# Performance work log

Measured on AMD Instinct MI355X. Metric: run time of the kernel, lower is better.

## Reference

```python
import jax, jax.numpy as jnp
import numpy as np

N_NODES = 50000
N_EDGES = 500000
D_FEAT = 128
OUT_CLASSES = 64


def setup_inputs() -> dict:
    key = jax.random.key(0)
    k_h, k_src, k_dst, k_w, k_b = jax.random.split(key, 5)
    h = jax.random.normal(k_h, (N_NODES, D_FEAT), dtype=jnp.float32)
    src = jax.random.randint(k_src, (N_EDGES,), 0, N_NODES, dtype=jnp.int64)
    dst = jax.random.randint(k_dst, (N_EDGES,), 0, N_NODES, dtype=jnp.int64)
    # nn.Linear(in_features*2, out_classes): weight [out, 2*in], bias [out]
    W = jax.random.normal(k_w, (OUT_CLASSES, 2 * D_FEAT), dtype=jnp.float32) * (1.0 / np.sqrt(2 * D_FEAT))
    b = jax.random.normal(k_b, (OUT_CLASSES,), dtype=jnp.float32) * 0.01
    return {"h": h, "src": src, "dst": dst, "W": W, "b": b}


def reference(h, src, dst, W, b):
    # Gather per-edge endpoint features, concat along feature dim, linear score.
    # Equivalent to torch: self.W(torch.cat([h[src], h[dst]], 1))
    h_u = h[src]                # [E, D]
    h_v = h[dst]                # [E, D]
    # Split W into src/dst halves to avoid materializing the concat:
    W_u, W_v = W[:, :D_FEAT], W[:, D_FEAT:]
    score = h_u @ W_u.T + h_v @ W_v.T + b   # [E, out_classes]
    return score
```

## Files before the change

kernel.cpp:

```cpp
#include <hip/hip_runtime.h>
#include <stdint.h>
#include <stddef.h>

constexpr int kNodes = 50000;
constexpr int kEdges = 500000;
constexpr int kD     = 128;
constexpr int kC     = 64;
constexpr int kK     = 256;

typedef __attribute__((ext_vector_type(8))) short  short8;
typedef __attribute__((ext_vector_type(4))) float  floatx4;

__device__ __forceinline__ unsigned short f2bf(float f) {
  union { float f; unsigned u; } v; v.f = f;
  unsigned u = v.u;
  unsigned r = u + 0x7FFFu + ((u >> 16) & 1u);
  return (unsigned short)(r >> 16);
}

__device__ __forceinline__ float bf2f(short s) {
  union { unsigned u; float f; } v;
  v.u = ((unsigned)(unsigned short)s) << 16;
  return v.f;
}

__device__ __forceinline__ short8 cvt8(floatx4 a, floatx4 b) {
  short8 r;
  r[0] = (short)f2bf(a[0]); r[1] = (short)f2bf(a[1]);
  r[2] = (short)f2bf(a[2]); r[3] = (short)f2bf(a[3]);
  r[4] = (short)f2bf(b[0]); r[5] = (short)f2bf(b[1]);
  r[6] = (short)f2bf(b[2]); r[7] = (short)f2bf(b[3]);
  return r;
}

__global__ __launch_bounds__(256)
void node_gemm_kernel(const float* __restrict__ h,
                      const float* __restrict__ W,
                      const float* __restrict__ b,
                      unsigned short* __restrict__ Pu,
                      unsigned short* __restrict__ Pv) {
  __shared__ short8 Blds[2048];

  const int tid = threadIdx.x;

  for (int s = tid; s < 2048; s += 256) {
    int kstep = s >> 9;
    int ntile = (s >> 6) & 7;
    int ln    = s & 63;
    int np = ntile * 16 + (ln & 15);
    int k  = kstep * 32 + (ln >> 4) * 8;
    int wc = (np < kC) ? np : (np - kC);
    int wk = (np < kC) ? k  : (k + kD);
    const float* wp = W + wc * kK + wk;
    Blds[s] = cvt8(*reinterpret_cast<const floatx4*>(wp),
                   *reinterpret_cast<const floatx4*>(wp + 4));
  }

  const int lane = tid & 63;
  const int wave = tid >> 6;
  const int rowA = lane & 15;
  const int quad = lane >> 4;
  const int col  = rowA;

  const int rowbase = blockIdx.x * 128 + wave * 32;
  int n0 = rowbase + rowA;       if (n0 >= kNodes) n0 = kNodes - 1;
  int n1 = rowbase + 16 + rowA;  if (n1 >= kNodes) n1 = kNodes - 1;

  short8 a0[4], a1[4];
#pragma unroll
  for (int kstep = 0; kstep < 4; ++kstep) {
    const float* p0 = h + (size_t)n0 * kD + kstep * 32 + quad * 8;
    const float* p1 = h + (size_t)n1 * kD + kstep * 32 + quad * 8;
    a0[kstep] = cvt8(__builtin_nontemporal_load(reinterpret_cast<const floatx4*>(p0)),
                     __builtin_nontemporal_load(reinterpret_cast<const floatx4*>(p0 + 4)));
    a1[kstep] = cvt8(__builtin_nontemporal_load(reinterpret_cast<const floatx4*>(p1)),
                     __builtin_nontemporal_load(reinterpret_cast<const floatx4*>(p1 + 4)));
  }

  floatx4 acc0[8], acc1[8];
#pragma unroll
  for (int nt = 0; nt < 8; ++nt) {
    acc0[nt] = (floatx4){0.f, 0.f, 0.f, 0.f};
    acc1[nt] = (floatx4){0.f, 0.f, 0.f, 0.f};
  }

  __syncthreads();

#pragma unroll
  for (int kstep = 0; kstep < 4; ++kstep) {
#pragma unroll
    for (int nt = 0; nt < 8; ++nt) {
      short8 bfrag = Blds[(kstep * 8 + nt) * 64 + lane];
      acc0[nt] = __builtin_amdgcn_mfma_f32_16x16x32_bf16(a0[kstep], bfrag,
                                                         acc0[nt], 0, 0, 0);
      acc1[nt] = __builtin_amdgcn_mfma_f32_16x16x32_bf16(a1[kstep], bfrag,
                                                         acc1[nt], 0, 0, 0);
    }
  }

  const bool full = (rowbase + 32) <= kNodes;
#pragma unroll
  for (int nt = 0; nt < 4; ++nt) {
    float bv = b[nt * 16 + col];
#pragma unroll
    for (int r = 0; r < 4; ++r) {
      int ra = rowbase + quad * 4 + r;
      int rb = ra + 16;
      if (full || ra < kNodes)
        Pu[(size_t)ra * kC + nt * 16 + col] = f2bf(acc0[nt][r] + bv);
      if (full || rb < kNodes)
        Pu[(size_t)rb * kC + nt * 16 + col] = f2bf(acc1[nt][r] + bv);
    }
  }
#pragma unroll
  for (int nt = 4; nt < 8; ++nt) {
#pragma unroll
    for (int r = 0; r < 4; ++r) {
      int ra = rowbase + quad * 4 + r;
      int rb = ra + 16;
      if (full || ra < kNodes)
        Pv[(size_t)ra * kC + (nt - 4) * 16 + col] = f2bf(acc0[nt][r]);
      if (full || rb < kNodes)
        Pv[(size_t)rb * kC + (nt - 4) * 16 + col] = f2bf(acc1[nt][r]);
    }
  }
}

__global__ __launch_bounds__(256)
void edge_combine_kernel(const unsigned short* __restrict__ Pu,
                         const unsigned short* __restrict__ Pv,
                         const int* __restrict__ src,
                         const int* __restrict__ dst,
                         float* __restrict__ out) {
  const int tid  = threadIdx.x;
  const int lane = tid & 63;
  const int g    = lane & 7;
  const int er8  = lane >> 3;
  const int wave = tid >> 6;
  const long wbase = (long)blockIdx.x * 256 + (long)wave * 64;

  long eown = wbase + lane;
  if (eown >= kEdges) eown = kEdges - 1;
  const int si_own = __builtin_nontemporal_load(src + eown);
  const int di_own = __builtin_nontemporal_load(dst + eown);

  int sg[8], dg[8];
#pragma unroll
  for (int j = 0; j < 8; ++j) {
    sg[j] = __shfl(si_own, j * 8 + er8, 64);
    dg[j] = __shfl(di_own, j * 8 + er8, 64);
  }

  short8 pu[8], pv[8];
#pragma unroll
  for (int j = 0; j < 8; ++j) {
    pu[j] = *reinterpret_cast<const short8*>(
        Pu + (((size_t)(unsigned)sg[j]) << 6) + g * 8);
    pv[j] = *reinterpret_cast<const short8*>(
        Pv + (((size_t)(unsigned)dg[j]) << 6) + g * 8);
  }

  const bool full = (wbase + 64) <= (long)kEdges;
#pragma unroll
  for (int j = 0; j < 8; ++j) {
    const long e = wbase + j * 8 + er8;
    floatx4 o0, o1;
    o0[0] = bf2f(pu[j][0]) + bf2f(pv[j][0]);
    o0[1] = bf2f(pu[j][1]) + bf2f(pv[j][1]);
    o0[2] = bf2f(pu[j][2]) + bf2f(pv[j][2]);
    o0[3] = bf2f(pu[j][3]) + bf2f(pv[j][3]);
    o1[0] = bf2f(pu[j][4]) + bf2f(pv[j][4]);
    o1[1] = bf2f(pu[j][5]) + bf2f(pv[j][5]);
    o1[2] = bf2f(pu[j][6]) + bf2f(pv[j][6]);
    o1[3] = bf2f(pu[j][7]) + bf2f(pv[j][7]);
    if (full || e < kEdges) {
      float* op = out + e * (long)kC + g * 8;
      __builtin_nontemporal_store(o0, reinterpret_cast<floatx4*>(op));
      __builtin_nontemporal_store(o1, reinterpret_cast<floatx4*>(op + 4));
    }
  }
}

extern "C" void kernel_launch(void* const* d_in, const int* in_sizes, int n_in,
                              void* d_out, int out_size, void* d_ws, size_t ws_size,
                              hipStream_t stream) {
  const float* h   = (const float*)d_in[0];
  const int*   src = (const int*)  d_in[1];
  const int*   dst = (const int*)  d_in[2];
  const float* W   = (const float*)d_in[3];
  const float* b   = (const float*)d_in[4];
  float*       out = (float*)d_out;

  const size_t tbl = (size_t)kNodes * kC * sizeof(unsigned short);
  unsigned short* Pu = (unsigned short*)d_ws;
  unsigned short* Pv = (unsigned short*)((char*)d_ws + tbl);

  const int gemm_grid = (kNodes + 127) / 128;
  const int edge_grid = (kEdges + 255) / 256;

  node_gemm_kernel<<<gemm_grid, 256, 0, stream>>>(h, W, b, Pu, Pv);
  edge_combine_kernel<<<edge_grid, 256, 0, stream>>>(Pu, Pv, src, dst, out);
}
```

Before: 191.6 us.

## Interleave Pu/Pv into one table, stage GEMM epilogue in LDS, halve rows per wave

Merges the two bf16 projection tables into one interleaved [node,128] table, so each node's source and destination halves share a 256-byte row. The GEMM epilogue now goes through a per-wave LDS tile and writes coalesced 16-byte stores instead of scattered 2-byte stores. Each wave now handles 16 rows instead of 32, so the grid doubles and there is more parallelism, at the cost of reloading B fragments from LDS for fewer rows. The edge gather still fetches two 128-byte segments per edge, now from one table with a larger stride.

```diff
diff --git a/kernel.cpp b/kernel.cpp
--- a/kernel.cpp
+++ b/kernel.cpp
@@ -7,6 +7,7 @@
 constexpr int kD     = 128;
 constexpr int kC     = 64;
 constexpr int kK     = 256;
+constexpr int kP     = 128;
 
 typedef __attribute__((ext_vector_type(8))) short  short8;
 typedef __attribute__((ext_vector_type(4))) float  floatx4;
@@ -37,9 +38,9 @@
 void node_gemm_kernel(const float* __restrict__ h,
                       const float* __restrict__ W,
                       const float* __restrict__ b,
-                      unsigned short* __restrict__ Pu,
-                      unsigned short* __restrict__ Pv) {
+                      unsigned short* __restrict__ P) {
   __shared__ short8 Blds[2048];
+  __shared__ __align__(16) unsigned short ep[4][16][136];
 
   const int tid = threadIdx.x;
 
@@ -56,33 +57,26 @@
                    *reinterpret_cast<const floatx4*>(wp + 4));
   }
 
-  const int lane = tid & 63;
-  const int wave = tid >> 6;
-  const int rowA = lane & 15;
-  const int quad = lane >> 4;
-  const int col  = rowA;
+  const int lane  = tid & 63;
+  const int wave  = tid >> 6;
+  const int rowA  = lane & 15;
+  const int quad  = lane >> 4;
+  const int col16 = rowA;
 
-  const int rowbase = blockIdx.x * 128 + wave * 32;
-  int n0 = rowbase + rowA;       if (n0 >= kNodes) n0 = kNodes - 1;
-  int n1 = rowbase + 16 + rowA;  if (n1 >= kNodes) n1 = kNodes - 1;
+  const int rowbase = blockIdx.x * 64 + wave * 16;
+  int n0 = rowbase + rowA;  if (n0 >= kNodes) n0 = kNodes - 1;
 
-  short8 a0[4], a1[4];
+  short8 a0[4];
 #pragma unroll
   for (int kstep = 0; kstep < 4; ++kstep) {
     const float* p0 = h + (size_t)n0 * kD + kstep * 32 + quad * 8;
-    const float* p1 = h + (size_t)n1 * kD + kstep * 32 + quad * 8;
     a0[kstep] = cvt8(__builtin_nontemporal_load(reinterpret_cast<const floatx4*>(p0)),
                      __builtin_nontemporal_load(reinterpret_cast<const floatx4*>(p0 + 4)));
-    a1[kstep] = cvt8(__builtin_nontemporal_load(reinterpret_cast<const floatx4*>(p1)),
-                     __builtin_nontemporal_load(reinterpret_cast<const floatx4*>(p1 + 4)));
   }
 
-  floatx4 acc0[8], acc1[8];
+  floatx4 acc[8];
 #pragma unroll
-  for (int nt = 0; nt < 8; ++nt) {
-    acc0[nt] = (floatx4){0.f, 0.f, 0.f, 0.f};
-    acc1[nt] = (floatx4){0.f, 0.f, 0.f, 0.f};
-  }
+  for (int nt = 0; nt < 8; ++nt) acc[nt] = (floatx4){0.f, 0.f, 0.f, 0.f};
 
   __syncthreads();
 
@@ -91,44 +85,40 @@
 #pragma unroll
     for (int nt = 0; nt < 8; ++nt) {
       short8 bfrag = Blds[(kstep * 8 + nt) * 64 + lane];
-      acc0[nt] = __builtin_amdgcn_mfma_f32_16x16x32_bf16(a0[kstep], bfrag,
-                                                         acc0[nt], 0, 0, 0);
-      acc1[nt] = __builtin_amdgcn_mfma_f32_16x16x32_bf16(a1[kstep], bfrag,
-                                                         acc1[nt], 0, 0, 0);
+      acc[nt] = __builtin_amdgcn_mfma_f32_16x16x32_bf16(a0[kstep], bfrag,
+                                                        acc[nt], 0, 0, 0);
     }
   }
 
-  const bool full = (rowbase + 32) <= kNodes;
 #pragma unroll
   for (int nt = 0; nt < 4; ++nt) {
-    float bv = b[nt * 16 + col];
+    float bv = b[nt * 16 + col16];
 #pragma unroll
-    for (int r = 0; r < 4; ++r) {
-      int ra = rowbase + quad * 4 + r;
-      int rb = ra + 16;
-      if (full || ra < kNodes)
-        Pu[(size_t)ra * kC + nt * 16 + col] = f2bf(acc0[nt][r] + bv);
-      if (full || rb < kNodes)
-        Pu[(size_t)rb * kC + nt * 16 + col] = f2bf(acc1[nt][r] + bv);
-    }
+    for (int r = 0; r < 4; ++r)
+      ep[wave][quad * 4 + r][nt * 16 + col16] = f2bf(acc[nt][r] + bv);
   }
 #pragma unroll
   for (int nt = 4; nt < 8; ++nt) {
 #pragma unroll
-    for (int r = 0; r < 4; ++r) {
-      int ra = rowbase + quad * 4 + r;
-      int rb = ra + 16;
-      if (full || ra < kNodes)
-        Pv[(size_t)ra * kC + (nt - 4) * 16 + col] = f2bf(acc0[nt][r]);
-      if (full || rb < kNodes)
-        Pv[(size_t)rb * kC + (nt - 4) * 16 + col] = f2bf(acc1[nt][r]);
+    for (int r = 0; r < 4; ++r)
+      ep[wave][quad * 4 + r][nt * 16 + col16] = f2bf(acc[nt][r]);
+  }
+
+#pragma unroll
+  for (int c = 0; c < 4; ++c) {
+    int i   = c * 64 + lane;
+    int row = i >> 4;
+    int g   = i & 15;
+    int grow = rowbase + row;
+    if (grow < kNodes) {
+      short8 v = *reinterpret_cast<const short8*>(&ep[wave][row][g * 8]);
+      *reinterpret_cast<short8*>(P + (size_t)grow * kP + g * 8) = v;
     }
   }
 }
 
 __global__ __launch_bounds__(256)
-void edge_combine_kernel(const unsigned short* __restrict__ Pu,
-                         const unsigned short* __restrict__ Pv,
+void edge_combine_kernel(const unsigned short* __restrict__ P,
                          const int* __restrict__ src,
                          const int* __restrict__ dst,
                          float* __restrict__ out) {
@@ -155,9 +145,9 @@
 #pragma unroll
   for (int j = 0; j < 8; ++j) {
     pu[j] = *reinterpret_cast<const short8*>(
-        Pu + (((size_t)(unsigned)sg[j]) << 6) + g * 8);
+        P + (((size_t)(unsigned)sg[j]) << 7) + g * 8);
     pv[j] = *reinterpret_cast<const short8*>(
-        Pv + (((size_t)(unsigned)dg[j]) << 6) + g * 8);
+        P + (((size_t)(unsigned)dg[j]) << 7) + 64 + g * 8);
   }
 
   const bool full = (wbase + 64) <= (long)kEdges;
@@ -191,13 +181,11 @@
   const float* b   = (const float*)d_in[4];
   float*       out = (float*)d_out;
 
-  const size_t tbl = (size_t)kNodes * kC * sizeof(unsigned short);
-  unsigned short* Pu = (unsigned short*)d_ws;
-  unsigned short* Pv = (unsigned short*)((char*)d_ws + tbl);
+  unsigned short* P = (unsigned short*)d_ws;
 
-  const int gemm_grid = (kNodes + 127) / 128;
+  const int gemm_grid = (kNodes + 63) / 64;
   const int edge_grid = (kEdges + 255) / 256;
 
-  node_gemm_kernel<<<gemm_grid, 256, 0, stream>>>(h, W, b, Pu, Pv);
-  edge_combine_kernel<<<edge_grid, 256, 0, stream>>>(Pu, Pv, src, dst, out);
+  node_gemm_kernel<<<gemm_grid, 256, 0, stream>>>(h, W, b, P);
+  edge_combine_kernel<<<edge_grid, 256, 0, stream>>>(P, src, dst, out);
 }
```

Result: faster. 185.8 us (-3.0%).
